# Performance work log

Hardware: AMD Instinct MI355X
Metric: run time of the kernel (lower is better)

Reference implementation:

```python
import jax, jax.numpy as jnp
import numpy as np

B, U = 64, 512          # batch, max_units
CORE, UNIT = 512, 256   # core_output_size, unit_embedding_size
HID, ACT = 1024, 12     # hidden_layer_size, ACTION_COUNT


def setup_inputs() -> dict:
    key = jax.random.key(0)
    ks = jax.random.split(key, 6)
    core_output = jax.random.normal(ks[0], (B, 1, CORE), dtype=jnp.float32)
    own_unit_embeddings = jax.random.normal(ks[1], (B, U, UNIT), dtype=jnp.float32)
    nr_units = jax.random.randint(ks[2], (B, 1), 0, U, dtype=jnp.int32)
    nr_own_flags = jax.random.randint(ks[3], (B, 1), 0, 64, dtype=jnp.int32)
    W1 = jax.random.normal(ks[4], (CORE + UNIT, HID), dtype=jnp.float32) * (1.0 / np.sqrt(CORE + UNIT))
    b1 = jnp.zeros((HID,), dtype=jnp.float32)
    W2 = jax.random.normal(ks[5], (HID, ACT), dtype=jnp.float32) * (1.0 / np.sqrt(HID))
    b2 = jnp.zeros((ACT,), dtype=jnp.float32)
    return {"core_output": core_output, "own_unit_embeddings": own_unit_embeddings,
            "nr_units": nr_units, "nr_own_flags": nr_own_flags,
            "W1": W1, "b1": b1, "W2": W2, "b2": b2}


def reference(core_output, own_unit_embeddings, nr_units, nr_own_flags, W1, b1, W2, b2):
    b, u, _ = own_unit_embeddings.shape
    # broadcast core output to every unit slot and concat along features: [B, U, UNIT+CORE]
    core_rep = jnp.broadcast_to(core_output, (b, u, core_output.shape[-1]))
    combined = jnp.concatenate([own_unit_embeddings, core_rep], axis=-1)
    autoregressive_embedding = jax.nn.relu(jnp.einsum('buf,fh->buh', combined, W1) + b1)
    logits = jnp.einsum('buh,ha->bua', autoregressive_embedding, W2) + b2
    action_probs = jax.nn.softmax(logits, axis=-1)
    # vectorized range mask: mask[i, f:n, :] = 1 else 1e-9
    idx = jnp.arange(u, dtype=nr_units.dtype)[None, :]        # [1, U]
    valid = (idx >= nr_own_flags) & (idx < nr_units)          # [B, U]
    mask = jnp.where(valid, 1.0, 1e-9).astype(action_probs.dtype)[:, :, None]
    return action_probs * mask, autoregressive_embedding
```

## Files before the change

### kernel.cpp

```cpp
#include <hip/hip_runtime.h>
#include <hip/hip_fp16.h>
#include <cstdint>

typedef unsigned short ushort_t;
typedef _Float16 f16x8 __attribute__((ext_vector_type(8)));
typedef float f32x4 __attribute__((ext_vector_type(4)));

#define M_TOT  32768
#define K_EMB  256
#define K_CORE 512
#define ACT    12

__device__ __forceinline__ unsigned int pack2h(float a, float b) {
    __half2 h = __floats2half2_rn(a, b);
    union { __half2 h2; unsigned int u; } v; v.h2 = h; return v.u;
}

__global__ __launch_bounds__(256) void transpose_k(const float* __restrict__ W1,
                                                   ushort_t* __restrict__ W1T) {
    __shared__ float tile[64][65];
    const int t = threadIdx.x;
    const int k0 = blockIdx.x * 64, n0 = blockIdx.y * 64;
    const int r = t >> 4, c4 = (t & 15) * 4;
#pragma unroll
    for (int p = 0; p < 4; ++p) {
        const int row = r + p * 16;
        const float4 v = *(const float4*)(W1 + (size_t)(k0 + row) * 1024 + n0 + c4);
        tile[row][c4 + 0] = v.x; tile[row][c4 + 1] = v.y;
        tile[row][c4 + 2] = v.z; tile[row][c4 + 3] = v.w;
    }
    __syncthreads();
#pragma unroll
    for (int p = 0; p < 4; ++p) {
        const int nrow = r + p * 16;
        uint2 o;
        o.x = pack2h(tile[c4 + 0][nrow], tile[c4 + 1][nrow]);
        o.y = pack2h(tile[c4 + 2][nrow], tile[c4 + 3][nrow]);
        *(uint2*)(W1T + (size_t)(n0 + nrow) * 256 + k0 + c4) = o;
    }
}

__global__ __launch_bounds__(256) void corepart_k(const float* __restrict__ core,
                                                  const float* __restrict__ W1,
                                                  const float* __restrict__ b1,
                                                  float* __restrict__ cp) {
    const int b = blockIdx.y;
    const int n = blockIdx.x * 256 + threadIdx.x;
    float s = b1[n];
    const float* cr = core + b * K_CORE;
    const float* wp = W1 + (size_t)K_EMB * 1024 + n;
#pragma unroll 8
    for (int k = 0; k < K_CORE; ++k)
        s += cr[k] * wp[(size_t)k * 1024];
    cp[b * 1024 + n] = s;
}

__global__ __launch_bounds__(256, 1) void fused_k(const float* __restrict__ emb,
                                                  const ushort_t* __restrict__ w1t,
                                                  const float* __restrict__ cp,
                                                  const float* __restrict__ W2,
                                                  const float* __restrict__ b2,
                                                  const int* __restrict__ nr_units,
                                                  const int* __restrict__ nr_flags,
                                                  float* __restrict__ out0,
                                                  float* __restrict__ out1) {
    __shared__ __align__(16) ushort_t Asl[128 * 32];
    __shared__ __align__(16) ushort_t Bsl[128 * 32];
    __shared__ __align__(16) float logitAcc[128][ACT];

    const int t = threadIdx.x;
    const int w = t >> 6, L = t & 63;
    const int wm = w >> 1, wn = w & 1;
    const int lane16 = L & 15, qd = L >> 4;
    const int m0 = blockIdx.x * 128;
    const int bb = m0 >> 9;

    const int c0 = w * 128 + L, c1 = c0 + 64;
    const int rA0 = c0 >> 2, g0 = c0 & 3;
    const int rA1 = c1 >> 2, g1 = c1 & 3;
    uint4* lA0 = (uint4*)&Asl[rA0 * 32 + ((g0 ^ ((rA0 >> 1) & 3)) << 3)];
    uint4* lA1 = (uint4*)&Asl[rA1 * 32 + ((g1 ^ ((rA1 >> 1) & 3)) << 3)];
    uint4* lB0 = (uint4*)&Bsl[rA0 * 32 + ((g0 ^ ((rA0 >> 1) & 3)) << 3)];
    uint4* lB1 = (uint4*)&Bsl[rA1 * 32 + ((g1 ^ ((rA1 >> 1) & 3)) << 3)];
    const float*    gA0 = emb + (size_t)(m0 + rA0) * K_EMB + g0 * 8;
    const float*    gA1 = emb + (size_t)(m0 + rA1) * K_EMB + g1 * 8;
    const ushort_t* gB0 = w1t + (size_t)rA0 * K_EMB + g0 * 8;
    const ushort_t* gB1 = w1t + (size_t)rA1 * K_EMB + g1 * 8;

    int aoff[4], boff[4];
#pragma unroll
    for (int i = 0; i < 4; ++i) {
        const int ra = wm * 64 + i * 16 + lane16;
        aoff[i] = ra * 32 + ((qd ^ ((ra >> 1) & 3)) << 3);
        const int rb = wn * 64 + i * 16 + lane16;
        boff[i] = rb * 32 + ((qd ^ ((rb >> 1) & 3)) << 3);
    }

    f32x4 acc[4][4];
#pragma unroll
    for (int mi = 0; mi < 4; ++mi)
#pragma unroll
        for (int ni = 0; ni < 4; ++ni) acc[mi][ni] = (f32x4){0.f, 0.f, 0.f, 0.f};
    f32x4 la_a[16], la_b[16], la_c[16];
#pragma unroll
    for (int i = 0; i < 16; ++i) {
        la_a[i] = (f32x4){0.f, 0.f, 0.f, 0.f};
        la_b[i] = (f32x4){0.f, 0.f, 0.f, 0.f};
        la_c[i] = (f32x4){0.f, 0.f, 0.f, 0.f};
    }

    float4 pa0l = *(const float4*)gA0, pa0h = *(const float4*)(gA0 + 4);
    float4 pa1l = *(const float4*)gA1, pa1h = *(const float4*)(gA1 + 4);
    uint4  pb0  = *(const uint4*)gB0,  pb1  = *(const uint4*)gB1;

    for (int it = 0; it < 64; ++it) {
        if (it) __syncthreads();
        uint4 av0, av1;
        av0.x = pack2h(pa0l.x, pa0l.y); av0.y = pack2h(pa0l.z, pa0l.w);
        av0.z = pack2h(pa0h.x, pa0h.y); av0.w = pack2h(pa0h.z, pa0h.w);
        av1.x = pack2h(pa1l.x, pa1l.y); av1.y = pack2h(pa1l.z, pa1l.w);
        av1.z = pack2h(pa1h.x, pa1h.y); av1.w = pack2h(pa1h.z, pa1h.w);
        *lA0 = av0; *lA1 = av1; *lB0 = pb0; *lB1 = pb1;
        __syncthreads();
        if (it < 63) {
            const int itn = it + 1;
            const int ksn = itn & 7, ntn = itn >> 3;
            const size_t ao = (size_t)(ksn * 32);
            const size_t bo = (size_t)ntn * 128 * K_EMB + ksn * 32;
            pa0l = *(const float4*)(gA0 + ao); pa0h = *(const float4*)(gA0 + ao + 4);
            pa1l = *(const float4*)(gA1 + ao); pa1h = *(const float4*)(gA1 + ao + 4);
            pb0 = *(const uint4*)(gB0 + bo);   pb1 = *(const uint4*)(gB1 + bo);
        }
        f16x8 af[4], bfr[4];
#pragma unroll
        for (int mi = 0; mi < 4; ++mi) af[mi] = *(const f16x8*)&Asl[aoff[mi]];
#pragma unroll
        for (int ni = 0; ni < 4; ++ni) bfr[ni] = *(const f16x8*)&Bsl[boff[ni]];
#pragma unroll
        for (int mi = 0; mi < 4; ++mi)
#pragma unroll
            for (int ni = 0; ni < 4; ++ni)
                acc[mi][ni] = __builtin_amdgcn_mfma_f32_16x16x32_f16(af[mi], bfr[ni], acc[mi][ni], 0, 0, 0);

        if ((it & 7) == 7) {
            const int nt = it >> 3;
            const int colb = nt * 128 + wn * 64 + lane16;
            float cpv[4]; f32x4 w2a[4], w2b[4], w2c[4];
#pragma unroll
            for (int ni = 0; ni < 4; ++ni) {
                const int cg = colb + ni * 16;
                cpv[ni] = cp[bb * 1024 + cg];
                const f32x4* wp = (const f32x4*)(W2 + (size_t)cg * ACT);
                w2a[ni] = wp[0]; w2b[ni] = wp[1]; w2c[ni] = wp[2];
            }
#pragma unroll
            for (int mi = 0; mi < 4; ++mi) {
#pragma unroll
                for (int r = 0; r < 4; ++r) {
                    const size_t m = (size_t)(m0 + wm * 64 + mi * 16 + qd * 4 + r);
                    float* orow = out1 + m * 1024 + colb;
#pragma unroll
                    for (int ni = 0; ni < 4; ++ni) {
                        float v = acc[mi][ni][r] + cpv[ni];
                        v = v > 0.f ? v : 0.f;
                        orow[ni * 16] = v;
                        la_a[mi * 4 + r] += w2a[ni] * v;
                        la_b[mi * 4 + r] += w2b[ni] * v;
                        la_c[mi * 4 + r] += w2c[ni] * v;
                    }
                }
#pragma unroll
                for (int ni = 0; ni < 4; ++ni) acc[mi][ni] = (f32x4){0.f, 0.f, 0.f, 0.f};
            }
        }
    }

#pragma unroll
    for (int i = 0; i < 16; ++i)
#pragma unroll
        for (int s = 1; s < 16; s <<= 1)
#pragma unroll
            for (int j = 0; j < 4; ++j) {
                la_a[i][j] += __shfl_xor(la_a[i][j], s, 64);
                la_b[i][j] += __shfl_xor(la_b[i][j], s, 64);
                la_c[i][j] += __shfl_xor(la_c[i][j], s, 64);
            }

    __syncthreads();
    if (wn == 0 && lane16 == 0) {
#pragma unroll
        for (int i = 0; i < 16; ++i) {
            const int row = wm * 64 + (i >> 2) * 16 + qd * 4 + (i & 3);
            f32x4* p = (f32x4*)&logitAcc[row][0];
            p[0] = la_a[i]; p[1] = la_b[i]; p[2] = la_c[i];
        }
    }
    __syncthreads();
    if (wn == 1 && lane16 == 0) {
#pragma unroll
        for (int i = 0; i < 16; ++i) {
            const int row = wm * 64 + (i >> 2) * 16 + qd * 4 + (i & 3);
            f32x4* p = (f32x4*)&logitAcc[row][0];
            p[0] += la_a[i]; p[1] += la_b[i]; p[2] += la_c[i];
        }
    }
    __syncthreads();

    if (t < 128) {
        float lg[ACT];
#pragma unroll
        for (int a = 0; a < ACT; ++a) lg[a] = logitAcc[t][a] + b2[a];
        float mx = lg[0];
#pragma unroll
        for (int a = 1; a < ACT; ++a) mx = fmaxf(mx, lg[a]);
        float s = 0.f;
#pragma unroll
        for (int a = 0; a < ACT; ++a) { lg[a] = __expf(lg[a] - mx); s += lg[a]; }
        const float inv = 1.f / s;
        const int m = m0 + t;
        const int u = m & 511;
        const float msk = (u >= nr_flags[bb] && u < nr_units[bb]) ? 1.0f : 1e-9f;
        f32x4* op = (f32x4*)(out0 + (size_t)m * ACT);
        f32x4 o0, o1, o2;
#pragma unroll
        for (int j = 0; j < 4; ++j) {
            o0[j] = lg[j] * inv * msk;
            o1[j] = lg[j + 4] * inv * msk;
            o2[j] = lg[j + 8] * inv * msk;
        }
        op[0] = o0; op[1] = o1; op[2] = o2;
    }
}

extern "C" void kernel_launch(void* const* d_in, const int* in_sizes, int n_in,
                              void* d_out, int out_size, void* d_ws, size_t ws_size,
                              hipStream_t stream) {
    const float* core   = (const float*)d_in[0];
    const float* emb    = (const float*)d_in[1];
    const int* nr_units = (const int*)d_in[2];
    const int* nr_flags = (const int*)d_in[3];
    const float* W1     = (const float*)d_in[4];
    const float* b1     = (const float*)d_in[5];
    const float* W2     = (const float*)d_in[6];
    const float* b2     = (const float*)d_in[7];

    float* out0 = (float*)d_out;
    float* out1 = out0 + (size_t)M_TOT * ACT;

    ushort_t* w1t = (ushort_t*)d_ws;
    float* cp = (float*)((char*)d_ws + (size_t)1024 * 256 * 2);

    transpose_k<<<dim3(4, 16), 256, 0, stream>>>(W1, w1t);
    corepart_k<<<dim3(4, 64), 256, 0, stream>>>(core, W1, b1, cp);
    fused_k<<<dim3(256), 256, 0, stream>>>(emb, w1t, cp, W2, b2, nr_units, nr_flags, out0, out1);
}
```

Before: 266.8 us.

## Keep full A tile resident in LDS, double-buffer W1 and halve block rows

The fused kernel now loads the whole 64x256 embedding tile into LDS once, instead of re-streaming and re-converting it for every N tile. The W1 slices are double-buffered so each step needs a single barrier. Blocks shrink to 64 rows, giving 512 blocks and two blocks per CU, and the MFMA operands are swapped so output rows store as contiguous float4 with nontemporal stores. The corepart kernel also gets four independent accumulators. The risks are a larger LDS footprint and tighter register limits under launch_bounds(256,2).

```diff
diff --git a/kernel.cpp b/kernel.cpp
--- a/kernel.cpp
+++ b/kernel.cpp
@@ -5,6 +5,7 @@
 typedef unsigned short ushort_t;
 typedef _Float16 f16x8 __attribute__((ext_vector_type(8)));
 typedef float f32x4 __attribute__((ext_vector_type(4)));
+typedef unsigned int u32x4 __attribute__((ext_vector_type(4)));
 
 #define M_TOT  32768
 #define K_EMB  256
@@ -46,16 +47,20 @@
                                                   float* __restrict__ cp) {
     const int b = blockIdx.y;
     const int n = blockIdx.x * 256 + threadIdx.x;
-    float s = b1[n];
     const float* cr = core + b * K_CORE;
     const float* wp = W1 + (size_t)K_EMB * 1024 + n;
-#pragma unroll 8
-    for (int k = 0; k < K_CORE; ++k)
-        s += cr[k] * wp[(size_t)k * 1024];
-    cp[b * 1024 + n] = s;
-}
-
-__global__ __launch_bounds__(256, 1) void fused_k(const float* __restrict__ emb,
+    float s0 = 0.f, s1 = 0.f, s2 = 0.f, s3 = 0.f;
+#pragma unroll 4
+    for (int k = 0; k < K_CORE; k += 4) {
+        s0 += cr[k + 0] * wp[(size_t)(k + 0) * 1024];
+        s1 += cr[k + 1] * wp[(size_t)(k + 1) * 1024];
+        s2 += cr[k + 2] * wp[(size_t)(k + 2) * 1024];
+        s3 += cr[k + 3] * wp[(size_t)(k + 3) * 1024];
+    }
+    cp[b * 1024 + n] = b1[n] + ((s0 + s1) + (s2 + s3));
+}
+
+__global__ __launch_bounds__(256, 2) void fused_k(const float* __restrict__ emb,
                                                   const ushort_t* __restrict__ w1t,
                                                   const float* __restrict__ cp,
                                                   const float* __restrict__ W2,
@@ -64,152 +69,154 @@
                                                   const int* __restrict__ nr_flags,
                                                   float* __restrict__ out0,
                                                   float* __restrict__ out1) {
-    __shared__ __align__(16) ushort_t Asl[128 * 32];
-    __shared__ __align__(16) ushort_t Bsl[128 * 32];
-    __shared__ __align__(16) float logitAcc[128][ACT];
+    __shared__ __align__(16) ushort_t Asl[64 * 256];
+    __shared__ __align__(16) ushort_t Bsl[2][128 * 32];
+    __shared__ __align__(16) float logitAcc[4][64][ACT];
 
     const int t = threadIdx.x;
     const int w = t >> 6, L = t & 63;
-    const int wm = w >> 1, wn = w & 1;
     const int lane16 = L & 15, qd = L >> 4;
-    const int m0 = blockIdx.x * 128;
-    const int bb = m0 >> 9;
-
-    const int c0 = w * 128 + L, c1 = c0 + 64;
-    const int rA0 = c0 >> 2, g0 = c0 & 3;
-    const int rA1 = c1 >> 2, g1 = c1 & 3;
-    uint4* lA0 = (uint4*)&Asl[rA0 * 32 + ((g0 ^ ((rA0 >> 1) & 3)) << 3)];
-    uint4* lA1 = (uint4*)&Asl[rA1 * 32 + ((g1 ^ ((rA1 >> 1) & 3)) << 3)];
-    uint4* lB0 = (uint4*)&Bsl[rA0 * 32 + ((g0 ^ ((rA0 >> 1) & 3)) << 3)];
-    uint4* lB1 = (uint4*)&Bsl[rA1 * 32 + ((g1 ^ ((rA1 >> 1) & 3)) << 3)];
-    const float*    gA0 = emb + (size_t)(m0 + rA0) * K_EMB + g0 * 8;
-    const float*    gA1 = emb + (size_t)(m0 + rA1) * K_EMB + g1 * 8;
-    const ushort_t* gB0 = w1t + (size_t)rA0 * K_EMB + g0 * 8;
-    const ushort_t* gB1 = w1t + (size_t)rA1 * K_EMB + g1 * 8;
-
-    int aoff[4], boff[4];
-#pragma unroll
-    for (int i = 0; i < 4; ++i) {
-        const int ra = wm * 64 + i * 16 + lane16;
-        aoff[i] = ra * 32 + ((qd ^ ((ra >> 1) & 3)) << 3);
-        const int rb = wn * 64 + i * 16 + lane16;
-        boff[i] = rb * 32 + ((qd ^ ((rb >> 1) & 3)) << 3);
-    }
-
-    f32x4 acc[4][4];
+    const int m0 = blockIdx.x * 64;
+    const int bb = blockIdx.x >> 3;
+
+    {
+        const int g = t & 31;
+        const int rsub = t >> 5;
+#pragma unroll
+        for (int p = 0; p < 8; ++p) {
+            const int r = p * 8 + rsub;
+            const float* src = emb + (size_t)(m0 + r) * K_EMB + g * 8;
+            const f32x4 v0 = __builtin_nontemporal_load((const f32x4*)src);
+            const f32x4 v1 = __builtin_nontemporal_load((const f32x4*)src + 1);
+            u32x4 pk;
+            pk[0] = pack2h(v0[0], v0[1]); pk[1] = pack2h(v0[2], v0[3]);
+            pk[2] = pack2h(v1[0], v1[1]); pk[3] = pack2h(v1[2], v1[3]);
+            *(u32x4*)((char*)Asl + r * 512 + ((g ^ (r & 7)) << 4)) = pk;
+        }
+    }
+
+    const int rB = t >> 2, gB = t & 3;
+    const ushort_t* gBa = w1t + (size_t)rB * K_EMB + gB * 8;
+    const int wb0 = rB * 64 + ((gB ^ ((rB >> 1) & 3)) << 4);
+    const int wb1 = wb0 + 64 * 64;
+
+    {
+        const u32x4 b0 = *(const u32x4*)gBa;
+        const u32x4 b1v = *(const u32x4*)(gBa + 64 * K_EMB);
+        *(u32x4*)((char*)Bsl + wb0) = b0;
+        *(u32x4*)((char*)Bsl + wb1) = b1v;
+    }
+    __syncthreads();
+
+    const int araw = lane16 * 512;
+    const int axor = lane16 & 7;
+    const int bswz = (qd ^ ((lane16 >> 1) & 3)) << 4;
+    int boffc[2];
+#pragma unroll
+    for (int ni = 0; ni < 2; ++ni)
+        boffc[ni] = (w * 32 + ni * 16 + lane16) * 64 + bswz;
+
+    f32x4 acc[2][4];
+#pragma unroll
+    for (int ni = 0; ni < 2; ++ni)
+#pragma unroll
+        for (int mi = 0; mi < 4; ++mi) acc[ni][mi] = (f32x4){0.f, 0.f, 0.f, 0.f};
+    f32x4 la[4][3];
 #pragma unroll
     for (int mi = 0; mi < 4; ++mi)
 #pragma unroll
-        for (int ni = 0; ni < 4; ++ni) acc[mi][ni] = (f32x4){0.f, 0.f, 0.f, 0.f};
-    f32x4 la_a[16], la_b[16], la_c[16];
-#pragma unroll
-    for (int i = 0; i < 16; ++i) {
-        la_a[i] = (f32x4){0.f, 0.f, 0.f, 0.f};
-        la_b[i] = (f32x4){0.f, 0.f, 0.f, 0.f};
-        la_c[i] = (f32x4){0.f, 0.f, 0.f, 0.f};
-    }
-
-    float4 pa0l = *(const float4*)gA0, pa0h = *(const float4*)(gA0 + 4);
-    float4 pa1l = *(const float4*)gA1, pa1h = *(const float4*)(gA1 + 4);
-    uint4  pb0  = *(const uint4*)gB0,  pb1  = *(const uint4*)gB1;
-
+        for (int c = 0; c < 3; ++c) la[mi][c] = (f32x4){0.f, 0.f, 0.f, 0.f};
+
+    u32x4 pb0, pb1;
+    int cur = 0;
     for (int it = 0; it < 64; ++it) {
-        if (it) __syncthreads();
-        uint4 av0, av1;
-        av0.x = pack2h(pa0l.x, pa0l.y); av0.y = pack2h(pa0l.z, pa0l.w);
-        av0.z = pack2h(pa0h.x, pa0h.y); av0.w = pack2h(pa0h.z, pa0h.w);
-        av1.x = pack2h(pa1l.x, pa1l.y); av1.y = pack2h(pa1l.z, pa1l.w);
-        av1.z = pack2h(pa1h.x, pa1h.y); av1.w = pack2h(pa1h.z, pa1h.w);
-        *lA0 = av0; *lA1 = av1; *lB0 = pb0; *lB1 = pb1;
-        __syncthreads();
+        const int ks = it & 7;
         if (it < 63) {
             const int itn = it + 1;
-            const int ksn = itn & 7, ntn = itn >> 3;
-            const size_t ao = (size_t)(ksn * 32);
-            const size_t bo = (size_t)ntn * 128 * K_EMB + ksn * 32;
-            pa0l = *(const float4*)(gA0 + ao); pa0h = *(const float4*)(gA0 + ao + 4);
-            pa1l = *(const float4*)(gA1 + ao); pa1h = *(const float4*)(gA1 + ao + 4);
-            pb0 = *(const uint4*)(gB0 + bo);   pb1 = *(const uint4*)(gB1 + bo);
-        }
-        f16x8 af[4], bfr[4];
-#pragma unroll
-        for (int mi = 0; mi < 4; ++mi) af[mi] = *(const f16x8*)&Asl[aoff[mi]];
-#pragma unroll
-        for (int ni = 0; ni < 4; ++ni) bfr[ni] = *(const f16x8*)&Bsl[boff[ni]];
+            const size_t off = (size_t)(itn >> 3) * 128 * K_EMB + (size_t)(itn & 7) * 32;
+            pb0 = *(const u32x4*)(gBa + off);
+            pb1 = *(const u32x4*)(gBa + 64 * K_EMB + off);
+        }
+        const int ga = (((ks << 2) | qd) ^ axor) << 4;
+        f16x8 af[4], bf[2];
 #pragma unroll
         for (int mi = 0; mi < 4; ++mi)
-#pragma unroll
-            for (int ni = 0; ni < 4; ++ni)
-                acc[mi][ni] = __builtin_amdgcn_mfma_f32_16x16x32_f16(af[mi], bfr[ni], acc[mi][ni], 0, 0, 0);
+            af[mi] = *(const f16x8*)((const char*)Asl + mi * 8192 + araw + ga);
+        const char* bbase = (const char*)Bsl + cur * 8192;
+#pragma unroll
+        for (int ni = 0; ni < 2; ++ni)
+            bf[ni] = *(const f16x8*)(bbase + boffc[ni]);
+#pragma unroll
+        for (int ni = 0; ni < 2; ++ni)
+#pragma unroll
+            for (int mi = 0; mi < 4; ++mi)
+                acc[ni][mi] = __builtin_amdgcn_mfma_f32_16x16x32_f16(bf[ni], af[mi], acc[ni][mi], 0, 0, 0);
 
         if ((it & 7) == 7) {
             const int nt = it >> 3;
-            const int colb = nt * 128 + wn * 64 + lane16;
-            float cpv[4]; f32x4 w2a[4], w2b[4], w2c[4];
-#pragma unroll
-            for (int ni = 0; ni < 4; ++ni) {
-                const int cg = colb + ni * 16;
-                cpv[ni] = cp[bb * 1024 + cg];
-                const f32x4* wp = (const f32x4*)(W2 + (size_t)cg * ACT);
-                w2a[ni] = wp[0]; w2b[ni] = wp[1]; w2c[ni] = wp[2];
-            }
-#pragma unroll
-            for (int mi = 0; mi < 4; ++mi) {
+#pragma unroll
+            for (int ni = 0; ni < 2; ++ni) {
+                const int nbase = nt * 128 + w * 32 + ni * 16 + qd * 4;
+                const f32x4 cpv = *(const f32x4*)(cp + bb * 1024 + nbase);
+#pragma unroll
+                for (int mi = 0; mi < 4; ++mi) {
+                    f32x4 v = acc[ni][mi] + cpv;
+#pragma unroll
+                    for (int j = 0; j < 4; ++j) v[j] = v[j] > 0.f ? v[j] : 0.f;
+                    acc[ni][mi] = v;
+                    const size_t m = (size_t)(m0 + mi * 16 + lane16);
+                    __builtin_nontemporal_store(v, (f32x4*)(out1 + m * 1024 + nbase));
+                }
 #pragma unroll
                 for (int r = 0; r < 4; ++r) {
-                    const size_t m = (size_t)(m0 + wm * 64 + mi * 16 + qd * 4 + r);
-                    float* orow = out1 + m * 1024 + colb;
-#pragma unroll
-                    for (int ni = 0; ni < 4; ++ni) {
-                        float v = acc[mi][ni][r] + cpv[ni];
-                        v = v > 0.f ? v : 0.f;
-                        orow[ni * 16] = v;
-                        la_a[mi * 4 + r] += w2a[ni] * v;
-                        la_b[mi * 4 + r] += w2b[ni] * v;
-                        la_c[mi * 4 + r] += w2c[ni] * v;
+                    const f32x4* wp = (const f32x4*)(W2 + (size_t)(nbase + r) * ACT);
+                    const f32x4 w2a = wp[0], w2b = wp[1], w2c = wp[2];
+#pragma unroll
+                    for (int mi = 0; mi < 4; ++mi) {
+                        const float vv = acc[ni][mi][r];
+                        la[mi][0] += w2a * vv;
+                        la[mi][1] += w2b * vv;
+                        la[mi][2] += w2c * vv;
                     }
                 }
 #pragma unroll
-                for (int ni = 0; ni < 4; ++ni) acc[mi][ni] = (f32x4){0.f, 0.f, 0.f, 0.f};
+                for (int mi = 0; mi < 4; ++mi) acc[ni][mi] = (f32x4){0.f, 0.f, 0.f, 0.f};
             }
         }
-    }
-
-#pragma unroll
-    for (int i = 0; i < 16; ++i)
-#pragma unroll
-        for (int s = 1; s < 16; s <<= 1)
+
+        if (it < 63) {
+            char* bnxt = (char*)Bsl + ((cur ^ 1) * 8192);
+            *(u32x4*)(bnxt + wb0) = pb0;
+            *(u32x4*)(bnxt + wb1) = pb1;
+        }
+        __syncthreads();
+        cur ^= 1;
+    }
+
+#pragma unroll
+    for (int mi = 0; mi < 4; ++mi)
+#pragma unroll
+        for (int c = 0; c < 3; ++c)
 #pragma unroll
             for (int j = 0; j < 4; ++j) {
-                la_a[i][j] += __shfl_xor(la_a[i][j], s, 64);
-                la_b[i][j] += __shfl_xor(la_b[i][j], s, 64);
-                la_c[i][j] += __shfl_xor(la_c[i][j], s, 64);
+                la[mi][c][j] += __shfl_xor(la[mi][c][j], 16, 64);
+                la[mi][c][j] += __shfl_xor(la[mi][c][j], 32, 64);
             }
-
+    if (L < 16) {
+#pragma unroll
+        for (int mi = 0; mi < 4; ++mi) {
+            f32x4* p = (f32x4*)&logitAcc[w][mi * 16 + L][0];
+            p[0] = la[mi][0]; p[1] = la[mi][1]; p[2] = la[mi][2];
+        }
+    }
     __syncthreads();
-    if (wn == 0 && lane16 == 0) {
-#pragma unroll
-        for (int i = 0; i < 16; ++i) {
-            const int row = wm * 64 + (i >> 2) * 16 + qd * 4 + (i & 3);
-            f32x4* p = (f32x4*)&logitAcc[row][0];
-            p[0] = la_a[i]; p[1] = la_b[i]; p[2] = la_c[i];
-        }
-    }
-    __syncthreads();
-    if (wn == 1 && lane16 == 0) {
-#pragma unroll
-        for (int i = 0; i < 16; ++i) {
-            const int row = wm * 64 + (i >> 2) * 16 + qd * 4 + (i & 3);
-            f32x4* p = (f32x4*)&logitAcc[row][0];
-            p[0] += la_a[i]; p[1] += la_b[i]; p[2] += la_c[i];
-        }
-    }
-    __syncthreads();
-
-    if (t < 128) {
+
+    if (t < 64) {
         float lg[ACT];
 #pragma unroll
-        for (int a = 0; a < ACT; ++a) lg[a] = logitAcc[t][a] + b2[a];
+        for (int a = 0; a < ACT; ++a)
+            lg[a] = logitAcc[0][t][a] + logitAcc[1][t][a]
+                  + logitAcc[2][t][a] + logitAcc[3][t][a] + b2[a];
         float mx = lg[0];
 #pragma unroll
         for (int a = 1; a < ACT; ++a) mx = fmaxf(mx, lg[a]);
@@ -220,7 +227,6 @@
         const int m = m0 + t;
         const int u = m & 511;
         const float msk = (u >= nr_flags[bb] && u < nr_units[bb]) ? 1.0f : 1e-9f;
-        f32x4* op = (f32x4*)(out0 + (size_t)m * ACT);
         f32x4 o0, o1, o2;
 #pragma unroll
         for (int j = 0; j < 4; ++j) {
@@ -228,7 +234,10 @@
             o1[j] = lg[j + 4] * inv * msk;
             o2[j] = lg[j + 8] * inv * msk;
         }
-        op[0] = o0; op[1] = o1; op[2] = o2;
+        f32x4* op = (f32x4*)(out0 + (size_t)m * ACT);
+        __builtin_nontemporal_store(o0, op + 0);
+        __builtin_nontemporal_store(o1, op + 1);
+        __builtin_nontemporal_store(o2, op + 2);
     }
 }
 
@@ -252,5 +261,5 @@
 
     transpose_k<<<dim3(4, 16), 256, 0, stream>>>(W1, w1t);
     corepart_k<<<dim3(4, 64), 256, 0, stream>>>(core, W1, b1, cp);
-    fused_k<<<dim3(256), 256, 0, stream>>>(emb, w1t, cp, W2, b2, nr_units, nr_flags, out0, out1);
-}
+    fused_k<<<dim3(512), 256, 0, stream>>>(emb, w1t, cp, W2, b2, nr_units, nr_flags, out0, out1);
+}
```

Result: faster. 243.1 us (-8.9%).
